# Kernel tuning notes

Measured on AMD Instinct MI355X. Metric: run time of the kernel, lower is better.

Reference implementation:

```python
import jax, jax.numpy as jnp
import numpy as np

D_MODEL = 2048
N_HEADS = 16
HEAD_DIM = D_MODEL // N_HEADS  # 128
SCALE_BASE = 512


def rotate_half(x):
    x1, x2 = jnp.split(x, 2, axis=-1)
    return jnp.concatenate((-x2, x1), axis=-1)


def rotary_xpos(seq_len, dim, dtype=jnp.float32):
    inv_freq = 1.0 / (10000.0 ** (jnp.arange(0, dim, 2, dtype=jnp.float32) / dim))
    t = jnp.arange(seq_len, dtype=jnp.float32)
    freqs = jnp.einsum('i,j->ij', t, inv_freq)
    freqs = jnp.concatenate((freqs, freqs), axis=-1)  # [S, dim]
    scale_base = (jnp.arange(0, dim, 2, dtype=jnp.float32) + 0.4 * dim) / (1.4 * dim)
    power = (t - seq_len // 2) / SCALE_BASE
    scale = scale_base[None, :] ** power[:, None]  # [S, dim/2]
    scale = jnp.concatenate((scale, scale), axis=-1)  # [S, dim]
    return freqs.astype(dtype), scale.astype(dtype)


def apply_rotary(t, pos, scale):
    return t * jnp.cos(pos) * scale + rotate_half(t) * jnp.sin(pos) * scale


def setup_inputs() -> dict:
    key = jax.random.key(0)
    ks = jax.random.split(key, 5)
    B, S = 2, 2048
    hidden_states = jax.random.normal(ks[0], (B, S, D_MODEL), dtype=jnp.float32)
    # Linear weights stored as [out, in] like torch; we use x @ W.T
    w_q = jax.random.normal(ks[1], (N_HEADS * HEAD_DIM, D_MODEL), dtype=jnp.float32) * 0.02
    w_kv = jax.random.normal(ks[2], (2 * HEAD_DIM, D_MODEL), dtype=jnp.float32) * 0.02
    w_proj = jax.random.normal(ks[3], (D_MODEL, N_HEADS * HEAD_DIM), dtype=jnp.float32) * 0.02
    b_proj = jax.random.normal(ks[4], (D_MODEL,), dtype=jnp.float32) * 0.02
    return {"hidden_states": hidden_states, "w_q": w_q, "w_kv": w_kv,
            "w_proj": w_proj, "b_proj": b_proj}


def reference(hidden_states, w_q, w_kv, w_proj, b_proj):
    B, S, _ = hidden_states.shape
    q = hidden_states @ w_q.T                      # [B,S,H*D]
    kv = hidden_states @ w_kv.T                    # [B,S,2*D]
    k, v = jnp.split(kv, 2, axis=-1)               # [B,S,D] each
    q = q.reshape(B, S, N_HEADS, HEAD_DIM).transpose(0, 2, 1, 3)  # [B,H,S,D]

    scale_w = HEAD_DIM ** (-0.5)
    q = q * scale_w
    k = k * scale_w

    pos, xscale = rotary_xpos(S, HEAD_DIM, q.dtype)
    q = apply_rotary(q, pos, xscale)               # broadcast [S,D] over [B,H,S,D]
    k = apply_rotary(k, pos, 1.0 / xscale)         # [B,S,D]

    attn = jnp.einsum('bnih,bjh->bnij', q, k)      # [B,H,S,S]
    causal = jnp.triu(jnp.ones((S, S), dtype=bool), 1)
    attn = jnp.where(causal, -jnp.finfo(attn.dtype).max, attn)
    attn = jax.nn.softmax(attn, axis=-1)

    out = jnp.einsum('bnij,bjd->bind', attn, v)    # [B,S,H,D]
    out = out.reshape(B, S, N_HEADS * HEAD_DIM)
    out = out @ w_proj.T + b_proj
    return out
```

## Files before the change

### kernel.cpp

```cpp
#include <hip/hip_runtime.h>
#include <math.h>

typedef __bf16 bf16;
typedef __bf16 bf16x8 __attribute__((ext_vector_type(8)));
typedef float f32x4 __attribute__((ext_vector_type(4)));
typedef float f32x16 __attribute__((ext_vector_type(16)));

#define MFMA16(a, b, c) __builtin_amdgcn_mfma_f32_16x16x32_bf16((a), (b), (c), 0, 0, 0)
#define MFMA32(a, b, c) __builtin_amdgcn_mfma_f32_32x32x16_bf16((a), (b), (c), 0, 0, 0)

__device__ __forceinline__ float clampf(float v, float lo, float hi) {
  return fminf(fmaxf(v, lo), hi);
}

__device__ __forceinline__ void async_copy16(const void* g, void* l) {
  __builtin_amdgcn_global_load_lds(
      (__attribute__((address_space(1))) void*)g,
      (__attribute__((address_space(3))) void*)l,
      16, 0, 0);
}

__device__ __forceinline__ unsigned cvtpk(float a, float b) {
  unsigned r;
  asm("v_cvt_pk_bf16_f32 %0, %1, %2" : "=v"(r) : "v"(a), "v"(b));
  return r;
}

__device__ __forceinline__ void pl32swap(unsigned& a, unsigned& b, int hi) {
#if __has_builtin(__builtin_amdgcn_permlane32_swap)
  auto r = __builtin_amdgcn_permlane32_swap(a, b, false, false);
  a = r[0];
  b = r[1];
#else
  unsigned ax = (unsigned)__shfl_xor((int)a, 32, 64);
  unsigned bx = (unsigned)__shfl_xor((int)b, 32, 64);
  unsigned o0 = hi ? bx : a;
  unsigned o1 = hi ? b : ax;
  a = o0; b = o1;
#endif
}

__device__ __forceinline__ bf16x8 frag4(unsigned d0, unsigned d1, unsigned d2, unsigned d3) {
  union { unsigned u[4]; bf16x8 v; } t;
  t.u[0] = d0; t.u[1] = d1; t.u[2] = d2; t.u[3] = d3;
  return t.v;
}


__global__ void convert_bf16(const float* __restrict__ hs,
                             const float* __restrict__ wq,
                             const float* __restrict__ wkv,
                             const float* __restrict__ wproj,
                             bf16* __restrict__ hs_bf,
                             bf16* __restrict__ wqkv_bf,
                             bf16* __restrict__ wproj_bf) {
  const long long v = (long long)blockIdx.x * blockDim.x + threadIdx.x;
  const float* src;
  bf16* dst;
  long long off;
  if (v < 1048576) { src = hs; dst = hs_bf; off = v; }
  else if (v < 1572864) { src = wq; dst = wqkv_bf; off = v - 1048576; }
  else if (v < 1638400) { src = wkv; dst = wqkv_bf + 4194304; off = v - 1572864; }
  else { src = wproj; dst = wproj_bf; off = v - 1638400; }
  const f32x4* p = (const f32x4*)(src + off * 8);
  f32x4 f0 = p[0], f1 = p[1];
  bf16x8 r;
#pragma unroll
  for (int i = 0; i < 4; ++i) { r[i] = (bf16)f0[i]; r[i + 4] = (bf16)f1[i]; }
  *(bf16x8*)(dst + off * 8) = r;
}

__global__ __launch_bounds__(256, 2)
void gemm_qkv(const bf16* __restrict__ A, const bf16* __restrict__ Bw,
              bf16* __restrict__ Cq, bf16* __restrict__ Ckv) {
  const int K = 2048;
  __shared__ bf16 As[128 * 32];
  __shared__ bf16 Bs[128 * 32];
  const int tid = threadIdx.x;
  const int wave = tid >> 6, lane = tid & 63;
  const int quad = lane >> 4, l15 = lane & 15;
  const int r4 = lane >> 2, c4 = lane & 3;
  const int wm = wave >> 1, wn = wave & 1;
  const int orig = blockIdx.x + 18 * blockIdx.y;
  const int wgid = (orig & 7) * 72 + (orig >> 3);
  const int bx = wgid % 18;
  const int bm = (wgid / 18) * 128;
  const bf16* Bp = Bw + (size_t)bx * 128 * K;

  const f32x4 vzero = {0.f, 0.f, 0.f, 0.f};
  f32x4 acc[4][4];
#pragma unroll
  for (int i = 0; i < 4; ++i)
#pragma unroll
    for (int j = 0; j < 4; ++j) acc[i][j] = vzero;

  for (int kt = 0; kt < K; kt += 32) {
    __syncthreads();
#pragma unroll
    for (int q = 0; q < 2; ++q) {
      const int chunk = wave * 2 + q;
      const int row = chunk * 16 + r4;
      async_copy16(A + (size_t)(bm + row) * K + kt + c4 * 8, (char*)As + chunk * 1024);
      async_copy16(Bp + (size_t)row * K + kt + c4 * 8, (char*)Bs + chunk * 1024);
    }
    __syncthreads();
    bf16x8 af[4], bfr[4];
#pragma unroll
    for (int i = 0; i < 4; ++i)
      af[i] = *(const bf16x8*)((const char*)As + (wm * 64 + i * 16 + l15) * 64 + quad * 16);
#pragma unroll
    for (int i = 0; i < 4; ++i)
      bfr[i] = *(const bf16x8*)((const char*)Bs + (wn * 64 + i * 16 + l15) * 64 + quad * 16);
#pragma unroll
    for (int mi = 0; mi < 4; ++mi)
#pragma unroll
      for (int ni = 0; ni < 4; ++ni)
        acc[mi][ni] = MFMA16(af[mi], bfr[ni], acc[mi][ni]);
  }

  bf16* Cp;
  int ldc, cn;
  if (bx < 16) { Cp = Cq; ldc = 2048; cn = bx * 128; }
  else { Cp = Ckv; ldc = 256; cn = (bx - 16) * 128; }
#pragma unroll
  for (int mi = 0; mi < 4; ++mi)
#pragma unroll
    for (int ni = 0; ni < 4; ++ni) {
      const int col = cn + wn * 64 + ni * 16 + l15;
#pragma unroll
      for (int r = 0; r < 4; ++r) {
        const int row = bm + wm * 64 + mi * 16 + quad * 4 + r;
        Cp[(size_t)row * ldc + col] = (bf16)clampf(acc[mi][ni][r], -1000.f, 1000.f);
      }
    }
}

__global__ __launch_bounds__(256, 2)
void gemm_proj(const bf16* __restrict__ A, const bf16* __restrict__ Bw,
               const float* __restrict__ bias, float* __restrict__ C) {
  const int K = 2048;
  __shared__ bf16 As[128 * 32];
  __shared__ bf16 Bs[128 * 32];
  const int tid = threadIdx.x;
  const int wave = tid >> 6, lane = tid & 63;
  const int quad = lane >> 4, l15 = lane & 15;
  const int r4 = lane >> 2, c4 = lane & 3;
  const int wm = wave >> 1, wn = wave & 1;
  const int orig = blockIdx.x + 16 * blockIdx.y;
  const int wgid = (orig & 7) * 64 + (orig >> 3);
  const int bn = (wgid % 16) * 128;
  const int bm = (wgid / 16) * 128;
  const bf16* Bp = Bw + (size_t)bn * K;

  const f32x4 vzero = {0.f, 0.f, 0.f, 0.f};
  f32x4 acc[4][4];
#pragma unroll
  for (int i = 0; i < 4; ++i)
#pragma unroll
    for (int j = 0; j < 4; ++j) acc[i][j] = vzero;

  for (int kt = 0; kt < K; kt += 32) {
    __syncthreads();
#pragma unroll
    for (int q = 0; q < 2; ++q) {
      const int chunk = wave * 2 + q;
      const int row = chunk * 16 + r4;
      async_copy16(A + (size_t)(bm + row) * K + kt + c4 * 8, (char*)As + chunk * 1024);
      async_copy16(Bp + (size_t)row * K + kt + c4 * 8, (char*)Bs + chunk * 1024);
    }
    __syncthreads();
    bf16x8 af[4], bfr[4];
#pragma unroll
    for (int i = 0; i < 4; ++i)
      af[i] = *(const bf16x8*)((const char*)As + (wm * 64 + i * 16 + l15) * 64 + quad * 16);
#pragma unroll
    for (int i = 0; i < 4; ++i)
      bfr[i] = *(const bf16x8*)((const char*)Bs + (wn * 64 + i * 16 + l15) * 64 + quad * 16);
#pragma unroll
    for (int mi = 0; mi < 4; ++mi)
#pragma unroll
      for (int ni = 0; ni < 4; ++ni)
        acc[mi][ni] = MFMA16(af[mi], bfr[ni], acc[mi][ni]);
  }

#pragma unroll
  for (int mi = 0; mi < 4; ++mi)
#pragma unroll
    for (int ni = 0; ni < 4; ++ni) {
      const int col = bn + wn * 64 + ni * 16 + l15;
      const float bv = bias[col];
#pragma unroll
      for (int r = 0; r < 4; ++r) {
        const int row = bm + wm * 64 + mi * 16 + quad * 4 + r;
        C[(size_t)row * 2048 + col] = clampf(acc[mi][ni][r] + bv, -1000.f, 1000.f);
      }
    }
}

__global__ void rotary_kernel(bf16* __restrict__ Cq, bf16* __restrict__ Ckv,
                              bf16* __restrict__ VT) {
  const int row = blockIdx.x;
  const int b = row >> 11, s = row & 2047;
  const int t = threadIdx.x;
  const float power = (float)(s - 1024) * (1.0f / 512.0f);
  const float scale_w = 0.08838834764831845f;
  const float k_if = 0.2076205059304679f;

  const int h = t >> 4;
  const int j0 = (t & 15) * 4;
  const size_t qbase = (size_t)row * 2048 + (size_t)h * 128;
#pragma unroll
  for (int u = 0; u < 4; ++u) {
    const int j = j0 + u;
    const float pos = (float)s * exp2f(-k_if * (float)j);
    const float c = cosf(pos), sn = sinf(pos);
    const float sb = ((float)(2 * j) + 51.2f) * (1.0f / 179.2f);
    const float xs = exp2f(power * log2f(sb));
    const float f = xs * scale_w;
    const float q1 = (float)Cq[qbase + j];
    const float q2 = (float)Cq[qbase + j + 64];
    Cq[qbase + j]      = (bf16)((q1 * c - q2 * sn) * f);
    Cq[qbase + j + 64] = (bf16)((q2 * c + q1 * sn) * f);
  }

  if (t < 64) {
    const int j = t;
    const float pos = (float)s * exp2f(-k_if * (float)j);
    const float c = cosf(pos), sn = sinf(pos);
    const float sb = ((float)(2 * j) + 51.2f) * (1.0f / 179.2f);
    const float xs = exp2f(power * log2f(sb));
    const float f = scale_w / xs;
    const size_t kvb = (size_t)row * 256;
    const float k1 = (float)Ckv[kvb + j];
    const float k2 = (float)Ckv[kvb + j + 64];
    Ckv[kvb + j]      = (bf16)((k1 * c - k2 * sn) * f);
    Ckv[kvb + j + 64] = (bf16)((k2 * c + k1 * sn) * f);
  } else if (t < 128) {
    const int d = (t - 64) * 2;
    const size_t kvb = (size_t)row * 256 + 128;
    VT[((size_t)b * 128 + d) * 2048 + s]     = Ckv[kvb + d];
    VT[((size_t)b * 128 + d + 1) * 2048 + s] = Ckv[kvb + d + 1];
  }
}

__global__ __launch_bounds__(128, 1)
void flash_attn(const bf16* __restrict__ Qp, const bf16* __restrict__ Kkv,
                const bf16* __restrict__ VT, bf16* __restrict__ O) {
  __shared__ bf16 Ks[2][64 * 128];
  __shared__ bf16 Vs[2][128 * 64];

  const int tid = threadIdx.x;
  const int wave = tid >> 6, lane = tid & 63;
  const int hi = lane >> 5, l31 = lane & 31, l15 = lane & 15, l7 = lane & 7;
  const int bh = blockIdx.x, b = bh >> 4, h = bh & 15;
  const int y = blockIdx.y;
  const int nkvA = y + 1;
  const int wrow = wave * 32;

  const bf16* Kb = Kkv + (size_t)b * 2048 * 256;
  const bf16* Vb = VT + (size_t)b * 128 * 2048;

  f32x16 sacc[2];
  f32x16 oacc[4];
  bf16x8 qb[8];
  float lacc;
  const f32x16 vz16 = {0.f, 0.f, 0.f, 0.f, 0.f, 0.f, 0.f, 0.f,
                       0.f, 0.f, 0.f, 0.f, 0.f, 0.f, 0.f, 0.f};

  auto load_q = [&](int q0) {
#pragma unroll
    for (int ks = 0; ks < 8; ++ks)
      qb[ks] = *(const bf16x8*)(Qp + ((size_t)(b * 2048 + q0 + wrow + l31)) * 2048 +
                                h * 128 + ks * 16 + hi * 8);
  };
  auto reset_acc = [&]() {
    lacc = 0.f;
#pragma unroll
    for (int nt = 0; nt < 4; ++nt) oacc[nt] = vz16;
  };

  auto stage = [&](int kv0, int buf) {
#pragma unroll
    for (int t = 0; t < 8; ++t) {
      const int ii = wave * 8 + t;
      const int kvr = ii * 4 + (lane >> 4);
      async_copy16(Kb + (size_t)(kv0 + kvr) * 256 + 8 * ((lane & 15) ^ (kvr & 15)),
                   (char*)Ks[buf] + ii * 1024);
    }
#pragma unroll
    for (int t = 0; t < 8; ++t) {
      const int jj = wave * 8 + t;
      const int dr = jj * 8 + (lane >> 3);
      async_copy16(Vb + (size_t)dr * 2048 + kv0 + 8 * ((lane & 7) ^ (dr & 7)),
                   (char*)Vs[buf] + jj * 1024);
    }
  };

  auto epilogue = [&](int q0) {
    const float lt = lacc + __shfl_xor(lacc, 32, 64);
    const float linv = 1.0f / lt;
    float li[16];
#pragma unroll
    for (int r = 0; r < 16; ++r)
      li[r] = __shfl(linv, (r & 3) + 8 * (r >> 2) + 4 * hi, 64);
#pragma unroll
    for (int nt = 0; nt < 4; ++nt)
#pragma unroll
      for (int r = 0; r < 16; ++r) {
        const int qr = (r & 3) + 8 * (r >> 2) + 4 * hi;
        const int s = q0 + wrow + qr;
        O[((size_t)(b * 2048 + s)) * 2048 + h * 128 + nt * 32 + l31] =
            (bf16)(oacc[nt][r] * li[r]);
      }
  };

  int q0 = y * 64;
  load_q(q0);
  reset_acc();
  stage(0, 0);

  for (int jt = 0; jt < 33; ++jt) {
    const int kv0 = (jt < nkvA ? jt : jt - nkvA) * 64;
    const int buf = jt & 1;
    __syncthreads();
    if (jt + 1 < 33) {
      const int njt = jt + 1;
      stage((njt < nkvA ? njt : njt - nkvA) * 64, buf ^ 1);
    }

    if (kv0 <= q0 + wrow + 31) {
      sacc[0] = vz16;
      sacc[1] = vz16;
      __builtin_amdgcn_s_setprio(1);
#pragma unroll
      for (int ks = 0; ks < 8; ++ks) {
        const int sl = ((2 * ks + hi) ^ l15) << 4;
        bf16x8 ka0 = *(const bf16x8*)((const char*)Ks[buf] + l31 * 256 + sl);
        bf16x8 ka1 = *(const bf16x8*)((const char*)Ks[buf] + (32 + l31) * 256 + sl);
        sacc[0] = MFMA32(ka0, qb[ks], sacc[0]);
        sacc[1] = MFMA32(ka1, qb[ks], sacc[1]);
      }
      __builtin_amdgcn_s_setprio(0);

      const int qg = q0 + wrow + l31;
      float p[32];
      if (kv0 + 63 > q0 + wrow) {
#pragma unroll
        for (int mt = 0; mt < 2; ++mt)
#pragma unroll
          for (int r = 0; r < 16; ++r) {
            const int kg = kv0 + mt * 32 + (r & 3) + 8 * (r >> 2) + 4 * hi;
            p[mt * 16 + r] = (kg > qg) ? 0.0f : __expf(sacc[mt][r]);
          }
      } else {
#pragma unroll
        for (int mt = 0; mt < 2; ++mt)
#pragma unroll
          for (int r = 0; r < 16; ++r)
            p[mt * 16 + r] = __expf(sacc[mt][r]);
      }
#pragma unroll
      for (int i = 0; i < 32; ++i) lacc += p[i];

      bf16x8 pa[4];
#pragma unroll
      for (int mt = 0; mt < 2; ++mt) {
        const int o = mt * 16;
        unsigned a0 = cvtpk(p[o + 0], p[o + 1]);
        unsigned b0 = cvtpk(p[o + 4], p[o + 5]);
        pl32swap(a0, b0, hi);
        unsigned a1 = cvtpk(p[o + 2], p[o + 3]);
        unsigned b1 = cvtpk(p[o + 6], p[o + 7]);
        pl32swap(a1, b1, hi);
        pa[mt * 2 + 0] = frag4(a0, a1, b0, b1);
        unsigned a2 = cvtpk(p[o + 8], p[o + 9]);
        unsigned b2 = cvtpk(p[o + 12], p[o + 13]);
        pl32swap(a2, b2, hi);
        unsigned a3 = cvtpk(p[o + 10], p[o + 11]);
        unsigned b3 = cvtpk(p[o + 14], p[o + 15]);
        pl32swap(a3, b3, hi);
        pa[mt * 2 + 1] = frag4(a2, a3, b2, b3);
      }

      __builtin_amdgcn_s_setprio(1);
#pragma unroll
      for (int ks = 0; ks < 4; ++ks) {
        const int sl = ((2 * ks + hi) ^ l7) << 4;
#pragma unroll
        for (int nt = 0; nt < 4; ++nt) {
          bf16x8 vb = *(const bf16x8*)((const char*)Vs[buf] + (nt * 32 + l31) * 128 + sl);
          oacc[nt] = MFMA32(pa[ks], vb, oacc[nt]);
        }
      }
      __builtin_amdgcn_s_setprio(0);
    }

    if (jt == nkvA - 1) {
      epilogue(q0);
      reset_acc();
      q0 = (31 - y) * 64;
      load_q(q0);
    }
  }
  epilogue(q0);
}

extern "C" void kernel_launch(void* const* d_in, const int* in_sizes, int n_in,
                              void* d_out, int out_size, void* d_ws, size_t ws_size,
                              hipStream_t stream) {
  const float* hs     = (const float*)d_in[0];
  const float* w_q    = (const float*)d_in[1];
  const float* w_kv   = (const float*)d_in[2];
  const float* w_proj = (const float*)d_in[3];
  const float* b_proj = (const float*)d_in[4];
  float* out = (float*)d_out;
  bf16* Qbuf  = (bf16*)d_out;
  bf16* hs_bf = (bf16*)((char*)d_out + 16777216);

  char* ws = (char*)d_ws;
  bf16* Ckv      = (bf16*)(ws);
  bf16* VT       = (bf16*)(ws + 2097152);
  bf16* AO       = (bf16*)(ws + 3145728);
  bf16* wqkv_bf  = (bf16*)(ws + 19922944);
  bf16* wproj_bf = (bf16*)(ws + 29360128);

  convert_bf16<<<dim3(8448), dim3(256), 0, stream>>>(hs, w_q, w_kv, w_proj,
                                                     hs_bf, wqkv_bf, wproj_bf);
  gemm_qkv<<<dim3(18, 32), dim3(256), 0, stream>>>(hs_bf, wqkv_bf, Qbuf, Ckv);
  rotary_kernel<<<dim3(4096), dim3(256), 0, stream>>>(Qbuf, Ckv, VT);
  flash_attn<<<dim3(32, 16), dim3(128), 0, stream>>>(Qbuf, Ckv, VT, AO);
  gemm_proj<<<dim3(16, 32), dim3(256), 0, stream>>>(AO, wproj_bf, b_proj, out);
}
```

Baseline: 288.0 us.

## Use 128-row query tiles with four waves per attention block

Flash attention blocks now own a single 128-row query tile processed by four waves instead of pairing two 64-row tiles across two waves for causal load balancing. The block index is remapped so that heavy and light tiles interleave, and K/V staging is split across four waves, sharing each loaded KV tile among more query rows. Launch bounds move to 256 threads with two blocks per CU to raise occupancy. Per-block work now varies with position, which can leave some CUs idle near the tail.

```diff
diff --git a/kernel.cpp b/kernel.cpp
--- a/kernel.cpp
+++ b/kernel.cpp
@@ -243,7 +243,7 @@
   }
 }
 
-__global__ __launch_bounds__(128, 1)
+__global__ __launch_bounds__(256, 2)
 void flash_attn(const bf16* __restrict__ Qp, const bf16* __restrict__ Kkv,
                 const bf16* __restrict__ VT, bf16* __restrict__ O) {
   __shared__ bf16 Ks[2][64 * 128];
@@ -253,8 +253,10 @@
   const int wave = tid >> 6, lane = tid & 63;
   const int hi = lane >> 5, l31 = lane & 31, l15 = lane & 15, l7 = lane & 7;
   const int bh = blockIdx.x, b = bh >> 4, h = bh & 15;
-  const int y = blockIdx.y;
-  const int nkvA = y + 1;
+  const int L = blockIdx.y;
+  const int y = (L < 8) ? L : 23 - L;
+  const int nkv = 2 * y + 2;
+  const int q0 = y * 128;
   const int wrow = wave * 32;
 
   const bf16* Kb = Kkv + (size_t)b * 2048 * 256;
@@ -263,70 +265,41 @@
   f32x16 sacc[2];
   f32x16 oacc[4];
   bf16x8 qb[8];
-  float lacc;
+  float lacc = 0.f;
   const f32x16 vz16 = {0.f, 0.f, 0.f, 0.f, 0.f, 0.f, 0.f, 0.f,
                        0.f, 0.f, 0.f, 0.f, 0.f, 0.f, 0.f, 0.f};
-
-  auto load_q = [&](int q0) {
-#pragma unroll
-    for (int ks = 0; ks < 8; ++ks)
-      qb[ks] = *(const bf16x8*)(Qp + ((size_t)(b * 2048 + q0 + wrow + l31)) * 2048 +
-                                h * 128 + ks * 16 + hi * 8);
-  };
-  auto reset_acc = [&]() {
-    lacc = 0.f;
-#pragma unroll
-    for (int nt = 0; nt < 4; ++nt) oacc[nt] = vz16;
-  };
+#pragma unroll
+  for (int nt = 0; nt < 4; ++nt) oacc[nt] = vz16;
+
+#pragma unroll
+  for (int ks = 0; ks < 8; ++ks)
+    qb[ks] = *(const bf16x8*)(Qp + ((size_t)(b * 2048 + q0 + wrow + l31)) * 2048 +
+                              h * 128 + ks * 16 + hi * 8);
 
   auto stage = [&](int kv0, int buf) {
 #pragma unroll
-    for (int t = 0; t < 8; ++t) {
-      const int ii = wave * 8 + t;
+    for (int t = 0; t < 4; ++t) {
+      const int ii = wave * 4 + t;
       const int kvr = ii * 4 + (lane >> 4);
       async_copy16(Kb + (size_t)(kv0 + kvr) * 256 + 8 * ((lane & 15) ^ (kvr & 15)),
                    (char*)Ks[buf] + ii * 1024);
     }
 #pragma unroll
-    for (int t = 0; t < 8; ++t) {
-      const int jj = wave * 8 + t;
+    for (int t = 0; t < 4; ++t) {
+      const int jj = wave * 4 + t;
       const int dr = jj * 8 + (lane >> 3);
       async_copy16(Vb + (size_t)dr * 2048 + kv0 + 8 * ((lane & 7) ^ (dr & 7)),
                    (char*)Vs[buf] + jj * 1024);
     }
   };
 
-  auto epilogue = [&](int q0) {
-    const float lt = lacc + __shfl_xor(lacc, 32, 64);
-    const float linv = 1.0f / lt;
-    float li[16];
-#pragma unroll
-    for (int r = 0; r < 16; ++r)
-      li[r] = __shfl(linv, (r & 3) + 8 * (r >> 2) + 4 * hi, 64);
-#pragma unroll
-    for (int nt = 0; nt < 4; ++nt)
-#pragma unroll
-      for (int r = 0; r < 16; ++r) {
-        const int qr = (r & 3) + 8 * (r >> 2) + 4 * hi;
-        const int s = q0 + wrow + qr;
-        O[((size_t)(b * 2048 + s)) * 2048 + h * 128 + nt * 32 + l31] =
-            (bf16)(oacc[nt][r] * li[r]);
-      }
-  };
-
-  int q0 = y * 64;
-  load_q(q0);
-  reset_acc();
   stage(0, 0);
 
-  for (int jt = 0; jt < 33; ++jt) {
-    const int kv0 = (jt < nkvA ? jt : jt - nkvA) * 64;
+  for (int jt = 0; jt < nkv; ++jt) {
+    const int kv0 = jt * 64;
     const int buf = jt & 1;
     __syncthreads();
-    if (jt + 1 < 33) {
-      const int njt = jt + 1;
-      stage((njt < nkvA ? njt : njt - nkvA) * 64, buf ^ 1);
-    }
+    if (jt + 1 < nkv) stage(kv0 + 64, buf ^ 1);
 
     if (kv0 <= q0 + wrow + 31) {
       sacc[0] = vz16;
@@ -394,15 +367,25 @@
       }
       __builtin_amdgcn_s_setprio(0);
     }
-
-    if (jt == nkvA - 1) {
-      epilogue(q0);
-      reset_acc();
-      q0 = (31 - y) * 64;
-      load_q(q0);
-    }
-  }
-  epilogue(q0);
+  }
+
+  {
+    const float lt = lacc + __shfl_xor(lacc, 32, 64);
+    const float linv = 1.0f / lt;
+    float li[16];
+#pragma unroll
+    for (int r = 0; r < 16; ++r)
+      li[r] = __shfl(linv, (r & 3) + 8 * (r >> 2) + 4 * hi, 64);
+#pragma unroll
+    for (int nt = 0; nt < 4; ++nt)
+#pragma unroll
+      for (int r = 0; r < 16; ++r) {
+        const int qr = (r & 3) + 8 * (r >> 2) + 4 * hi;
+        const int s = q0 + wrow + qr;
+        O[((size_t)(b * 2048 + s)) * 2048 + h * 128 + nt * 32 + l31] =
+            (bf16)(oacc[nt][r] * li[r]);
+      }
+  }
 }
 
 extern "C" void kernel_launch(void* const* d_in, const int* in_sizes, int n_in,
@@ -428,6 +411,6 @@
                                                      hs_bf, wqkv_bf, wproj_bf);
   gemm_qkv<<<dim3(18, 32), dim3(256), 0, stream>>>(hs_bf, wqkv_bf, Qbuf, Ckv);
   rotary_kernel<<<dim3(4096), dim3(256), 0, stream>>>(Qbuf, Ckv, VT);
-  flash_attn<<<dim3(32, 16), dim3(128), 0, stream>>>(Qbuf, Ckv, VT, AO);
+  flash_attn<<<dim3(32, 16), dim3(256), 0, stream>>>(Qbuf, Ckv, VT, AO);
   gemm_proj<<<dim3(16, 32), dim3(256), 0, stream>>>(AO, wproj_bf, b_proj, out);
 }
```

Result: faster. 276.3 us (-4.1%).
